# Kernel tuning notes

Hardware: AMD Instinct MI355X
Metric: run time of the kernel (lower is better)

Reference implementation:

```python
import jax, jax.numpy as jnp
import numpy as np

B, S, D_MODEL, H_DIM = 8, 4096, 512, 120  # h = 1, so d_k = h_dim = 120
NEG_INF = jnp.float32(-1e9)
L2_EPS = 1e-12  # F.normalize eps


def setup_inputs() -> dict:
    key = jax.random.key(0)
    k_q, k_m, k_w, k_wt = jax.random.split(key, 4)
    query = jax.random.normal(k_q, (B, S, D_MODEL), dtype=jnp.float32)
    mask = jax.random.randint(k_m, (B, S, S), 0, 2, dtype=jnp.int32)
    # q_linear params (kaiming-uniform-ish init scale)
    lim = 1.0 / np.sqrt(D_MODEL)
    w_q = jax.random.uniform(k_w, (H_DIM, D_MODEL), jnp.float32, -lim, lim)
    b_q = jnp.zeros((H_DIM,), jnp.float32)
    # weight_tensor: shape (h, d_k) = (1, 120), xavier-uniform scale
    wt_lim = np.sqrt(6.0 / (1 + H_DIM))
    weight_tensor = jax.random.uniform(k_wt, (1, H_DIM), jnp.float32, -wt_lim, wt_lim)
    return {"query": query, "mask": mask, "w_q": w_q, "b_q": b_q,
            "weight_tensor": weight_tensor}


def reference(query, mask, w_q, b_q, weight_tensor):
    # context = q_linear(query).view(B, -1, h_dim); with h=1 the view is identity
    context = jnp.einsum("bsd,kd->bsk", query, w_q) + b_q          # [B, S, 120]
    # weighted then L2-normalized (cosine-similarity) features
    ctx = context * weight_tensor[:, None, :]                        # bcast (1,1,120)
    norm = jnp.sqrt(jnp.sum(ctx * ctx, axis=-1, keepdims=True))
    ctx_n = ctx / jnp.maximum(norm, L2_EPS)
    scores = jnp.einsum("bqk,bpk->bqp", ctx_n, ctx_n)               # [B, S, S]
    scores = jnp.where(mask == 0, NEG_INF, scores)                   # masked_fill
    return jax.nn.softmax(scores, axis=-1)                           # dropout: eval/identity
```

## Files before the change

kernel.cpp:

```cpp
#include <hip/hip_runtime.h>
#include <hip/hip_bf16.h>
#include <stdint.h>

#define BATCH 8
#define SEQ   4096
#define DM    512
#define HD    120
#define PH    2048
#define NT    32

typedef __bf16   v8bf  __attribute__((ext_vector_type(8)));
typedef float    v4f   __attribute__((ext_vector_type(4)));
typedef int      i4    __attribute__((ext_vector_type(4)));
typedef uint32_t u32x2 __attribute__((ext_vector_type(2)));
typedef uint32_t u32x4 __attribute__((ext_vector_type(4)));
typedef float    f32x4 __attribute__((ext_vector_type(4)));

static __device__ __forceinline__ ushort f2bf(float x) {
  uint32_t u = __builtin_bit_cast(uint32_t, x);
  return (ushort)((u + 0x7fffu + ((u >> 16) & 1u)) >> 16);
}

__global__ __launch_bounds__(256) void prep_kernel(
    const float* __restrict__ q, const float* __restrict__ wq,
    const float* __restrict__ bq, const float* __restrict__ wt,
    const int* __restrict__ mask, ushort* __restrict__ ctx,
    uint32_t* __restrict__ bitsT)
{
  __shared__ __align__(16) char smem[33024];
  const int t = threadIdx.x;

  if (blockIdx.x & 1) {
    uint32_t (*bw)[129] = (uint32_t(*)[129])smem;
    const int cb = blockIdx.x >> 1;
    const size_t row0 = (size_t)cb * 64;
    const int b     = (int)(row0 >> 12);
    const int qbase = (int)(row0 & 4095);
    const int rhalf = t >> 7, pw = t & 127;
    for (int s = 0; s < 32; ++s) {
      int row = s * 2 + rhalf;
      const int* mp = mask + (row0 + row) * SEQ + pw * 32;
      uint32_t wd = 0;
      #pragma unroll
      for (int k = 0; k < 8; ++k) {
        i4 m = *(const i4*)(mp + k * 4);
        wd |= (uint32_t)(m.x != 0) << (k * 4);
        wd |= (uint32_t)(m.y != 0) << (k * 4 + 1);
        wd |= (uint32_t)(m.z != 0) << (k * 4 + 2);
        wd |= (uint32_t)(m.w != 0) << (k * 4 + 3);
      }
      bw[row][pw] = wd;
    }
    __syncthreads();
    const int qq = t & 63, pg = t >> 6;
    uint32_t* bT = bitsT + (size_t)b * 128 * 4096 + qbase + qq;
    #pragma unroll 8
    for (int i = 0; i < 32; ++i) {
      int pw2 = pg * 32 + i;
      bT[(size_t)pw2 * 4096] = bw[qq][pw2];
    }
    return;
  }

  float (*qs)[68]   = (float(*)[68])smem;
  float (*ws2)[136] = (float(*)[136])(smem + 8704);
  const int gb = blockIdx.x >> 1;
  const int tx = t & 31, ty = t >> 5;
  const size_t row0 = (size_t)gb * 64;
  const int qr = t >> 2, qk = (t & 3) * 8;

  float acc[8][4];
  #pragma unroll
  for (int j = 0; j < 8; ++j)
    #pragma unroll
    for (int i = 0; i < 4; ++i) acc[j][i] = 0.f;

  for (int k0 = 0; k0 < DM; k0 += 32) {
    __syncthreads();
    {
      f32x4 v0 = *(const f32x4*)&q[(row0 + qr) * DM + k0 + qk];
      f32x4 v1 = *(const f32x4*)&q[(row0 + qr) * DM + k0 + qk + 4];
      #pragma unroll
      for (int i = 0; i < 4; ++i) qs[qk + i][qr] = v0[i];
      #pragma unroll
      for (int i = 0; i < 4; ++i) qs[qk + 4 + i][qr] = v1[i];
    }
    #pragma unroll
    for (int i = 0; i < 16; ++i) {
      int flat = t + i * 256;
      int kk = flat & 31, c = flat >> 5;
      ws2[kk][c] = (c < HD) ? wq[c * DM + k0 + kk] : 0.f;
    }
    __syncthreads();
    #pragma unroll
    for (int kk = 0; kk < 32; ++kk) {
      f32x4 bv = *(const f32x4*)&ws2[kk][tx * 4];
      f32x4 a0 = *(const f32x4*)&qs[kk][ty * 8];
      f32x4 a1 = *(const f32x4*)&qs[kk][ty * 8 + 4];
      #pragma unroll
      for (int r = 0; r < 4; ++r)
        #pragma unroll
        for (int c = 0; c < 4; ++c) {
          acc[r][c]     = fmaf(a0[r], bv[c], acc[r][c]);
          acc[4 + r][c] = fmaf(a1[r], bv[c], acc[4 + r][c]);
        }
    }
  }

  float wtv[4], bqv[4];
  #pragma unroll
  for (int i = 0; i < 4; ++i) {
    int c = tx * 4 + i;
    wtv[i] = (c < HD) ? wt[c] : 0.f;
    bqv[i] = (c < HD) ? bq[c] : 0.f;
  }
  #pragma unroll
  for (int j = 0; j < 8; ++j) {
    int r = ty * 8 + j;
    float v[4]; float ss = 0.f;
    #pragma unroll
    for (int i = 0; i < 4; ++i) {
      v[i] = (acc[j][i] + bqv[i]) * wtv[i];
      ss = fmaf(v[i], v[i], ss);
    }
    #pragma unroll
    for (int xm = 1; xm < 32; xm <<= 1) ss += __shfl_xor(ss, xm, 64);
    float rinv = 1.f / fmaxf(sqrtf(ss), 1e-12f);
    uint32_t p0 = (uint32_t)f2bf(v[0] * rinv) | ((uint32_t)f2bf(v[1] * rinv) << 16);
    uint32_t p1 = (uint32_t)f2bf(v[2] * rinv) | ((uint32_t)f2bf(v[3] * rinv) << 16);
    u32x2 o = {p0, p1};
    char* dst = (char*)ctx + (row0 + r) * 256 +
                (((tx >> 1) * 16) ^ ((r & 7) << 4)) + (tx & 1) * 8;
    *(u32x2*)dst = o;
  }
}

#define MFMA(A, B, C) __builtin_amdgcn_mfma_f32_16x16x32_bf16(A, B, C, 0, 0, 0)

static __device__ __forceinline__ v8bf ldfrag(const char* base, int row, int slot) {
  int byte = row * 256 + ((slot * 16) ^ ((row & 7) << 4));
  return __builtin_bit_cast(v8bf, *(const u32x4*)(base + byte));
}

#define STG_LOAD(R, j) do {                                                   \
  const char* _g = ctxb + (size_t)(P0 + (j) * 64) * 256 + w * 4096 + lane * 16;\
  R##0 = *(const u32x4*)(_g);        R##1 = *(const u32x4*)(_g + 1024);       \
  R##2 = *(const u32x4*)(_g + 2048); R##3 = *(const u32x4*)(_g + 3072);       \
} while (0)

#define STG_WRITE(R, buf) do {                                                \
  char* _l = (buf) + w * 4096 + lane * 16;                                    \
  *(u32x4*)(_l)        = R##0;  *(u32x4*)(_l + 1024) = R##1;                  \
  *(u32x4*)(_l + 2048) = R##2;  *(u32x4*)(_l + 3072) = R##3;                  \
} while (0)

#define QKT(buf, acc) do {                                                    \
  _Pragma("unroll")                                                           \
  for (int _t = 0; _t < 4; ++_t) {                                            \
    acc[_t] = (v4f){0.f, 0.f, 0.f, 0.f};                                      \
    _Pragma("unroll")                                                         \
    for (int _k = 0; _k < 4; ++_k) {                                          \
      v8bf _a = ldfrag(buf, _t * 16 + ln, _k * 4 + g);                        \
      acc[_t] = MFMA(_a, qf[_k], acc[_t]);                                    \
    }                                                                         \
  }                                                                           \
} while (0)

#define LDB(x, y, tj) do {                                                    \
  x = btb[(size_t)(tj) * 2 * 4096];                                           \
  y = btb[((size_t)(tj) * 2 + 1) * 4096];                                     \
} while (0)

#define EPIA() do {                                                           \
  _Pragma("unroll")                                                           \
  for (int _t2 = 0; _t2 < 4; ++_t2) {                                         \
    uint32_t nib = ((_t2 < 2 ? bcx : bcy) >> ((_t2 & 1) * 16 + g * 4));       \
    _Pragma("unroll")                                                         \
    for (int _i = 0; _i < 4; ++_i) {                                          \
      float e = __expf(acc[_t2][_i] - 1.0f);                                  \
      lsum += ((nib >> _i) & 1u) ? e : 0.f;                                   \
    }                                                                         \
  }                                                                           \
} while (0)

#define EPIB(tj) do {                                                         \
  _Pragma("unroll")                                                           \
  for (int _t2 = 0; _t2 < 4; ++_t2) {                                         \
    uint32_t nib = ((_t2 < 2 ? bcx : bcy) >> ((_t2 & 1) * 16 + g * 4));       \
    f32x4 o;                                                                  \
    _Pragma("unroll")                                                         \
    for (int _i = 0; _i < 4; ++_i)                                            \
      o[_i] = ((nib >> _i) & 1u) ? __expf(acc[_t2][_i] - 1.0f) * lir : 0.f;   \
    *(f32x4*)(orow + (size_t)(tj) * 64 + _t2 * 16 + g * 4) = o;               \
  }                                                                           \
} while (0)

#define BAR() do {                                                            \
  asm volatile("s_waitcnt lgkmcnt(0)" ::: "memory");                          \
  __builtin_amdgcn_s_barrier();                                               \
  __builtin_amdgcn_sched_barrier(0);                                          \
} while (0)

#define ATTN_COMMON                                                           \
  __shared__ __align__(16) char lds[32768];                                   \
  char* B0 = lds;                                                             \
  char* B1 = lds + 16384;                                                     \
  const int t    = threadIdx.x;                                               \
  const int b    = blockIdx.x & 7;                                            \
  const int rest = blockIdx.x >> 3;                                           \
  const int ph   = rest & 1;                                                  \
  const int qg   = rest >> 1;                                                 \
  const int w    = t >> 6, lane = t & 63;                                     \
  const int ln   = lane & 15, g = lane >> 4;                                  \
  const int q0   = qg * 64;                                                   \
  const int P0   = ph * PH;                                                   \
  const int qrow = q0 + w * 16 + ln;                                          \
  const char* ctxb = (const char*)ctx + (size_t)b * SEQ * 256;                \
  const uint32_t* __restrict__ btb =                                          \
      bitsT + ((size_t)b * 128 + (P0 >> 5)) * 4096 + qrow;                    \
  v8bf qf[4];                                                                 \
  _Pragma("unroll")                                                           \
  for (int kk = 0; kk < 4; ++kk) {                                            \
    int slot = kk * 4 + g;                                                    \
    qf[kk] = *(const v8bf*)(ctxb + (size_t)qrow * 256 +                       \
                            ((slot * 16) ^ ((qrow & 7) << 4)));               \
  }                                                                           \
  u32x4 sA0, sA1, sA2, sA3, sB0, sB1, sB2, sB3;                               \
  uint32_t bcx, bcy, bnx = 0, bny = 0;

__global__ __launch_bounds__(256) void attnA_kernel(
    const ushort* __restrict__ ctx, const uint32_t* __restrict__ bitsT,
    float* __restrict__ lpart)
{
  ATTN_COMMON
  float lsum = 0.f;

  STG_LOAD(sA, 0);
  STG_WRITE(sA, B0);
  STG_LOAD(sB, 1);
  LDB(bcx, bcy, 0);
  __syncthreads();

  for (int jj = 0; jj < NT; jj += 2) {
    if (jj + 1 < NT) LDB(bnx, bny, jj + 1);
    if (jj + 2 < NT) STG_LOAD(sA, jj + 2);
    { v4f acc[4]; QKT(B0, acc); STG_WRITE(sB, B1); EPIA(); }
    BAR();
    bcx = bnx; bcy = bny;

    if (jj + 2 < NT) LDB(bnx, bny, jj + 2);
    if (jj + 3 < NT) STG_LOAD(sB, jj + 3);
    { v4f acc[4]; QKT(B1, acc); if (jj + 2 < NT) STG_WRITE(sA, B0); EPIA(); }
    BAR();
    bcx = bnx; bcy = bny;
  }

  lsum += __shfl_xor(lsum, 16, 64);
  lsum += __shfl_xor(lsum, 32, 64);
  if (g == 0)
    lpart[(size_t)ph * (BATCH * SEQ) + (size_t)b * SEQ + qrow] = lsum;
}

__global__ __launch_bounds__(256) void attnB_kernel(
    const ushort* __restrict__ ctx, const uint32_t* __restrict__ bitsT,
    const float* __restrict__ lpart, float* __restrict__ out)
{
  ATTN_COMMON
  const size_t grow = (size_t)b * SEQ + qrow;
  const float lf = lpart[grow] + lpart[(size_t)(BATCH * SEQ) + grow];
  const float lir = (lf > 0.f) ? (1.f / lf) : 0.f;
  float* __restrict__ orow = out + grow * SEQ + P0;

  STG_LOAD(sA, 0);
  STG_WRITE(sA, B0);
  STG_LOAD(sB, 1);
  LDB(bcx, bcy, 0);
  __syncthreads();

  for (int jj = 0; jj < NT; jj += 2) {
    if (jj + 1 < NT) LDB(bnx, bny, jj + 1);
    if (jj + 2 < NT) STG_LOAD(sA, jj + 2);
    { v4f acc[4]; QKT(B0, acc); STG_WRITE(sB, B1); EPIB(jj); }
    BAR();
    bcx = bnx; bcy = bny;

    if (jj + 2 < NT) LDB(bnx, bny, jj + 2);
    if (jj + 3 < NT) STG_LOAD(sB, jj + 3);
    { v4f acc[4]; QKT(B1, acc); if (jj + 2 < NT) STG_WRITE(sA, B0); EPIB(jj + 1); }
    BAR();
    bcx = bnx; bcy = bny;
  }
}

extern "C" void kernel_launch(void* const* d_in, const int* in_sizes, int n_in,
                              void* d_out, int out_size, void* d_ws, size_t ws_size,
                              hipStream_t stream) {
  const float* query = (const float*)d_in[0];
  const int*   mask  = (const int*)d_in[1];
  const float* w_q   = (const float*)d_in[2];
  const float* b_q   = (const float*)d_in[3];
  const float* wt    = (const float*)d_in[4];
  float* out = (float*)d_out;

  ushort*   ctx   = (ushort*)d_ws;
  uint32_t* bitsT = (uint32_t*)((char*)d_ws + (9u << 20));
  float*    lpart = (float*)((char*)d_ws + (26u << 20));

  prep_kernel <<<dim3(1024), dim3(256), 0, stream>>>(query, w_q, b_q, wt, mask, ctx, bitsT);
  attnA_kernel<<<dim3(1024), dim3(256), 0, stream>>>(ctx, bitsT, lpart);
  attnB_kernel<<<dim3(1024), dim3(256), 0, stream>>>(ctx, bitsT, lpart, out);
}
```

Before: 394.7 us.

## Compute Q projection with split-bf16 MFMA instead of scalar FP32 FMAs

Replaces the FP32 FMA GEMM for the query projection with bf16 MFMA using a hi/lo split (three MFMAs per tile) to keep near-FP32 accuracy. A new small kernel pre-splits W_q into bf16 hi/lo arrays in workspace, and the epilogue is remapped to the MFMA output layout. This targets the compute cost of the projection half of prep_kernel, at the price of an extra kernel launch and scattered 2-byte stores to ctx.

```diff
diff --git a/kernel.cpp b/kernel.cpp
--- a/kernel.cpp
+++ b/kernel.cpp
@@ -20,12 +20,33 @@
   uint32_t u = __builtin_bit_cast(uint32_t, x);
   return (ushort)((u + 0x7fffu + ((u >> 16) & 1u)) >> 16);
 }
+static __device__ __forceinline__ float bf2f(ushort h) {
+  return __builtin_bit_cast(float, (uint32_t)h << 16);
+}
+
+__global__ __launch_bounds__(256) void wsplit_kernel(
+    const float* __restrict__ wq, ushort* __restrict__ whi,
+    ushort* __restrict__ wlo)
+{
+  int base = (blockIdx.x * 256 + threadIdx.x) * 4;
+  #pragma unroll
+  for (int j = 0; j < 4; ++j) {
+    int e = base + j;
+    int col = e >> 9;
+    float w = (col < HD) ? wq[e - (col << 9) + col * DM] : 0.f;
+    ushort h = f2bf(w);
+    whi[e] = h;
+    wlo[e] = f2bf(w - bf2f(h));
+  }
+}
+
+#define MFMA(A, B, C) __builtin_amdgcn_mfma_f32_16x16x32_bf16(A, B, C, 0, 0, 0)
 
 __global__ __launch_bounds__(256) void prep_kernel(
-    const float* __restrict__ q, const float* __restrict__ wq,
-    const float* __restrict__ bq, const float* __restrict__ wt,
-    const int* __restrict__ mask, ushort* __restrict__ ctx,
-    uint32_t* __restrict__ bitsT)
+    const float* __restrict__ q, const float* __restrict__ bq,
+    const float* __restrict__ wt, const int* __restrict__ mask,
+    const ushort* __restrict__ whi, const ushort* __restrict__ wlo,
+    ushort* __restrict__ ctx, uint32_t* __restrict__ bitsT)
 {
   __shared__ __align__(16) char smem[33024];
   const int t = threadIdx.x;
@@ -62,80 +83,97 @@
     return;
   }
 
-  float (*qs)[68]   = (float(*)[68])smem;
-  float (*ws2)[136] = (float(*)[136])(smem + 8704);
+  ushort* AHI = (ushort*)smem;
+  ushort* ALO = AHI + 64 * 40;
+  ushort* BHI = ALO + 64 * 40;
+  ushort* BLO = BHI + 128 * 40;
+
   const int gb = blockIdx.x >> 1;
-  const int tx = t & 31, ty = t >> 5;
   const size_t row0 = (size_t)gb * 64;
-  const int qr = t >> 2, qk = (t & 3) * 8;
-
-  float acc[8][4];
+  const int w = t >> 6, lane = t & 63;
+  const int ln = lane & 15, g = lane >> 4;
+
+  v4f acc[8];
   #pragma unroll
-  for (int j = 0; j < 8; ++j)
-    #pragma unroll
-    for (int i = 0; i < 4; ++i) acc[j][i] = 0.f;
-
-  for (int k0 = 0; k0 < DM; k0 += 32) {
+  for (int c = 0; c < 8; ++c) acc[c] = (v4f){0.f, 0.f, 0.f, 0.f};
+
+  const int srow = t >> 2, sk0 = (t & 3) * 8;
+  const int bcol = t & 127, bpl = t >> 7;
+  const ushort* bsrc = (bpl ? wlo : whi) + bcol * DM;
+  ushort* bdst = (bpl ? BLO : BHI) + bcol * 40;
+
+  for (int kc = 0; kc < 16; ++kc) {
     __syncthreads();
     {
-      f32x4 v0 = *(const f32x4*)&q[(row0 + qr) * DM + k0 + qk];
-      f32x4 v1 = *(const f32x4*)&q[(row0 + qr) * DM + k0 + qk + 4];
+      f32x4 v0 = *(const f32x4*)&q[(row0 + srow) * DM + kc * 32 + sk0];
+      f32x4 v1 = *(const f32x4*)&q[(row0 + srow) * DM + kc * 32 + sk0 + 4];
+      ushort h[8], l[8];
       #pragma unroll
-      for (int i = 0; i < 4; ++i) qs[qk + i][qr] = v0[i];
+      for (int i = 0; i < 4; ++i) {
+        h[i] = f2bf(v0[i]); l[i] = f2bf(v0[i] - bf2f(h[i]));
+        h[4 + i] = f2bf(v1[i]); l[4 + i] = f2bf(v1[i] - bf2f(h[4 + i]));
+      }
+      u32x4 ph, pl;
       #pragma unroll
-      for (int i = 0; i < 4; ++i) qs[qk + 4 + i][qr] = v1[i];
-    }
+      for (int i = 0; i < 4; ++i) {
+        ph[i] = (uint32_t)h[2 * i] | ((uint32_t)h[2 * i + 1] << 16);
+        pl[i] = (uint32_t)l[2 * i] | ((uint32_t)l[2 * i + 1] << 16);
+      }
+      *(u32x4*)&AHI[srow * 40 + sk0] = ph;
+      *(u32x4*)&ALO[srow * 40 + sk0] = pl;
+    }
+    {
+      const ushort* s = bsrc + kc * 32;
+      *(u32x4*)&bdst[0]  = *(const u32x4*)&s[0];
+      *(u32x4*)&bdst[8]  = *(const u32x4*)&s[8];
+      *(u32x4*)&bdst[16] = *(const u32x4*)&s[16];
+      *(u32x4*)&bdst[24] = *(const u32x4*)&s[24];
+    }
+    __syncthreads();
+
+    v8bf ah = *(const v8bf*)&AHI[(w * 16 + ln) * 40 + g * 8];
+    v8bf al = *(const v8bf*)&ALO[(w * 16 + ln) * 40 + g * 8];
     #pragma unroll
-    for (int i = 0; i < 16; ++i) {
-      int flat = t + i * 256;
-      int kk = flat & 31, c = flat >> 5;
-      ws2[kk][c] = (c < HD) ? wq[c * DM + k0 + kk] : 0.f;
-    }
-    __syncthreads();
-    #pragma unroll
-    for (int kk = 0; kk < 32; ++kk) {
-      f32x4 bv = *(const f32x4*)&ws2[kk][tx * 4];
-      f32x4 a0 = *(const f32x4*)&qs[kk][ty * 8];
-      f32x4 a1 = *(const f32x4*)&qs[kk][ty * 8 + 4];
-      #pragma unroll
-      for (int r = 0; r < 4; ++r)
-        #pragma unroll
-        for (int c = 0; c < 4; ++c) {
-          acc[r][c]     = fmaf(a0[r], bv[c], acc[r][c]);
-          acc[4 + r][c] = fmaf(a1[r], bv[c], acc[4 + r][c]);
-        }
-    }
-  }
-
-  float wtv[4], bqv[4];
+    for (int c = 0; c < 8; ++c) {
+      v8bf bh = *(const v8bf*)&BHI[(c * 16 + ln) * 40 + g * 8];
+      v8bf bl = *(const v8bf*)&BLO[(c * 16 + ln) * 40 + g * 8];
+      acc[c] = MFMA(ah, bh, acc[c]);
+      acc[c] = MFMA(ah, bl, acc[c]);
+      acc[c] = MFMA(al, bh, acc[c]);
+    }
+  }
+
+  float wtv[8], bqv[8];
+  #pragma unroll
+  for (int c = 0; c < 8; ++c) {
+    int col = c * 16 + ln;
+    wtv[c] = (col < HD) ? wt[col] : 0.f;
+    bqv[c] = (col < HD) ? bq[col] : 0.f;
+  }
   #pragma unroll
   for (int i = 0; i < 4; ++i) {
-    int c = tx * 4 + i;
-    wtv[i] = (c < HD) ? wt[c] : 0.f;
-    bqv[i] = (c < HD) ? bq[c] : 0.f;
-  }
-  #pragma unroll
-  for (int j = 0; j < 8; ++j) {
-    int r = ty * 8 + j;
-    float v[4]; float ss = 0.f;
+    int row = w * 16 + g * 4 + i;
+    float v[8]; float ss = 0.f;
     #pragma unroll
-    for (int i = 0; i < 4; ++i) {
-      v[i] = (acc[j][i] + bqv[i]) * wtv[i];
-      ss = fmaf(v[i], v[i], ss);
-    }
+    for (int c = 0; c < 8; ++c) {
+      v[c] = (acc[c][i] + bqv[c]) * wtv[c];
+      ss = fmaf(v[c], v[c], ss);
+    }
+    ss += __shfl_xor(ss, 1, 64);
+    ss += __shfl_xor(ss, 2, 64);
+    ss += __shfl_xor(ss, 4, 64);
+    ss += __shfl_xor(ss, 8, 64);
+    float rinv = 1.f / fmaxf(sqrtf(ss), 1e-12f);
+    char* rbase = (char*)ctx + (row0 + row) * 256;
+    int rx = (row & 7) << 4;
     #pragma unroll
-    for (int xm = 1; xm < 32; xm <<= 1) ss += __shfl_xor(ss, xm, 64);
-    float rinv = 1.f / fmaxf(sqrtf(ss), 1e-12f);
-    uint32_t p0 = (uint32_t)f2bf(v[0] * rinv) | ((uint32_t)f2bf(v[1] * rinv) << 16);
-    uint32_t p1 = (uint32_t)f2bf(v[2] * rinv) | ((uint32_t)f2bf(v[3] * rinv) << 16);
-    u32x2 o = {p0, p1};
-    char* dst = (char*)ctx + (row0 + r) * 256 +
-                (((tx >> 1) * 16) ^ ((r & 7) << 4)) + (tx & 1) * 8;
-    *(u32x2*)dst = o;
-  }
-}
-
-#define MFMA(A, B, C) __builtin_amdgcn_mfma_f32_16x16x32_bf16(A, B, C, 0, 0, 0)
+    for (int c = 0; c < 8; ++c) {
+      int col = c * 16 + ln;
+      *(ushort*)(rbase + (((col >> 3) * 16) ^ rx) + (col & 7) * 2)
+          = f2bf(v[c] * rinv);
+    }
+  }
+}
 
 static __device__ __forceinline__ v8bf ldfrag(const char* base, int row, int slot) {
   int byte = row * 256 + ((slot * 16) ^ ((row & 7) << 4));
@@ -303,10 +341,14 @@
   float* out = (float*)d_out;
 
   ushort*   ctx   = (ushort*)d_ws;
+  ushort*   whi   = (ushort*)((char*)d_ws + (8u << 20));
+  ushort*   wlo   = (ushort*)((char*)d_ws + (8u << 20) + (128u << 10));
   uint32_t* bitsT = (uint32_t*)((char*)d_ws + (9u << 20));
   float*    lpart = (float*)((char*)d_ws + (26u << 20));
 
-  prep_kernel <<<dim3(1024), dim3(256), 0, stream>>>(query, w_q, b_q, wt, mask, ctx, bitsT);
-  attnA_kernel<<<dim3(1024), dim3(256), 0, stream>>>(ctx, bitsT, lpart);
-  attnB_kernel<<<dim3(1024), dim3(256), 0, stream>>>(ctx, bitsT, lpart, out);
-}
+  wsplit_kernel<<<dim3(64),   dim3(256), 0, stream>>>(w_q, whi, wlo);
+  prep_kernel  <<<dim3(1024), dim3(256), 0, stream>>>(query, b_q, wt, mask,
+                                                      whi, wlo, ctx, bitsT);
+  attnA_kernel <<<dim3(1024), dim3(256), 0, stream>>>(ctx, bitsT, lpart);
+  attnB_kernel <<<dim3(1024), dim3(256), 0, stream>>>(ctx, bitsT, lpart, out);
+}
```

Result: no change. 402.3 us (+1.9%).
